# Kernel tuning notes

Measured on AMD Instinct MI355X. Metric: run time of the kernel, lower is better.

Reference implementation:

```python
import jax, jax.numpy as jnp
import numpy as np

NEG = -1.0e9  # large negative number used for causal masking in the original


def setup_inputs() -> dict:
    key = jax.random.key(0)
    ks = jax.random.split(key, 9)
    B, S, D, H = 4, 4096, 512, 64
    sd = 1.0 / np.sqrt(D)
    sh = 1.0 / np.sqrt(H)
    return {
        "x": jax.random.normal(ks[0], (B, S, D), jnp.float32),
        # nn.Linear(d_model, d_head): stored here as (in, out) matrices
        "Wq": jax.random.normal(ks[1], (D, H), jnp.float32) * sd,
        "bq": jax.random.normal(ks[2], (H,), jnp.float32) * 0.01,
        "Wk": jax.random.normal(ks[3], (D, H), jnp.float32) * sd,
        "bk": jax.random.normal(ks[4], (H,), jnp.float32) * 0.01,
        "Wv": jax.random.normal(ks[5], (D, H), jnp.float32) * sd,
        "bv": jax.random.normal(ks[6], (H,), jnp.float32) * 0.01,
        "Wo": jax.random.normal(ks[7], (H, D), jnp.float32) * sh,
        "bo": jax.random.normal(ks[8], (D,), jnp.float32) * 0.01,
    }


def reference(x, Wq, bq, Wk, bk, Wv, bv, Wo, bo):
    # x: (B, S, D)
    B, S, D = x.shape
    Q = x @ Wq + bq  # (B, S, H)
    K = x @ Wk + bk
    V = x @ Wv + bv
    scores = jnp.einsum("bsh,bth->bst", Q, K)  # (B, S, S)
    # NOTE: original divides by sqrt(scores.shape[-1]) == sqrt(seq_len), not sqrt(d_head)
    scores = scores / jnp.sqrt(jnp.asarray(S, scores.dtype))
    # causal mask: strictly-upper-triangular entries get NEG added
    mask = jnp.triu(jnp.full((S, S), NEG, dtype=scores.dtype), k=1)
    attn = jax.nn.softmax(scores + mask[None, :, :], axis=-1)
    out = jnp.einsum("bst,bth->bsh", attn, V)  # (B, S, H)
    return out @ Wo + bo  # (B, S, D)
```

## Files before the change

### kernel.cpp

```cpp
#include <hip/hip_runtime.h>

#define S_LEN 4096
#define NROWS 16384

typedef __attribute__((ext_vector_type(8))) __bf16 bf16x8;
typedef __attribute__((ext_vector_type(8))) unsigned short ushort8;
typedef __attribute__((ext_vector_type(4))) unsigned short ushort4_t;
typedef __attribute__((ext_vector_type(4))) float floatx4;

__device__ __forceinline__ unsigned short f2bf(float f) {
    union { __bf16 h; unsigned short u; } c;
    c.h = (__bf16)f;
    return c.u;
}

__device__ __forceinline__ float fexp2(float x) {
#if __has_builtin(__builtin_amdgcn_exp2f)
    return __builtin_amdgcn_exp2f(x);
#else
    float r; asm("v_exp_f32 %0, %1" : "=v"(r) : "v"(x)); return r;
#endif
}

__global__ __launch_bounds__(256) void convw_kernel(
    const float* __restrict__ Wq, const float* __restrict__ Wk,
    const float* __restrict__ Wv, const float* __restrict__ Wo,
    unsigned short* __restrict__ WqF, unsigned short* __restrict__ WkF,
    unsigned short* __restrict__ WvF, unsigned short* __restrict__ WoF)
{
    int tid = blockIdx.x * 256 + threadIdx.x;
    {
        const int e = tid & 7, cl = (tid >> 3) & 15, quad = (tid >> 7) & 3;
        const int kc = (tid >> 9) & 15, t = tid >> 13;
        const int n = t * 16 + cl, k = kc * 32 + quad * 8 + e;
        WqF[tid] = f2bf(Wq[k * 64 + n]);
        WkF[tid] = f2bf(Wk[k * 64 + n]);
        WvF[tid] = f2bf(Wv[k * 64 + n]);
    }
    {
        const int e = tid & 7, cl = (tid >> 3) & 15, quad = (tid >> 7) & 3;
        const int h = (tid >> 9) & 1, g = tid >> 10;
        const int n = g * 16 + cl, k = h * 32 + quad * 8 + e;
        WoF[tid] = f2bf(Wo[k * 512 + n]);
    }
}

__global__ __launch_bounds__(192) void qkv_kernel(
    const float* __restrict__ x,
    const unsigned short* __restrict__ WqF, const unsigned short* __restrict__ WkF,
    const unsigned short* __restrict__ WvF,
    const float* __restrict__ bq, const float* __restrict__ bk, const float* __restrict__ bv,
    unsigned short* __restrict__ Qb, unsigned short* __restrict__ KF,
    unsigned short* __restrict__ VF)
{
    __shared__ unsigned short xs[8192];
    const int row0 = blockIdx.x * 16;
    const int tid = threadIdx.x;

    const float* xt = x + (size_t)row0 * 512;
    for (int i = tid; i < 2048; i += 192) {
        float4 v = *(const float4*)(xt + i * 4);
        const int r = i >> 7, k = (i & 127) * 4;
        ushort4_t o;
        o[0] = f2bf(v.x); o[1] = f2bf(v.y); o[2] = f2bf(v.z); o[3] = f2bf(v.w);
        *(ushort4_t*)(xs + (k >> 5) * 512 + ((k >> 3) & 3) * 128 + r * 8 + (k & 7)) = o;
    }
    __syncthreads();

    const int m = tid >> 6;
    const int lane = tid & 63, cl = lane & 15, quad = lane >> 4;
    const unsigned short* WF = (m == 0) ? WqF : (m == 1) ? WkF : WvF;
    const float* bias = (m == 0) ? bq : (m == 1) ? bk : bv;

    floatx4 acc[4];
    #pragma unroll
    for (int t = 0; t < 4; t++) acc[t] = (floatx4){0.f, 0.f, 0.f, 0.f};
    #pragma unroll 2
    for (int kc = 0; kc < 16; kc++) {
        const bf16x8 af = *(const bf16x8*)(const void*)(xs + kc * 512 + lane * 8);
        #pragma unroll
        for (int t = 0; t < 4; t++) {
            const bf16x8 bf = *(const bf16x8*)(const void*)(WF + (size_t)(t * 16 + kc) * 512 + lane * 8);
            acc[t] = __builtin_amdgcn_mfma_f32_16x16x32_bf16(af, bf, acc[t], 0, 0, 0);
        }
    }
    if (m == 0) {
        const float scl = 0.022542110013890054f;
        #pragma unroll
        for (int t = 0; t < 4; t++) {
            const int d = t * 16 + cl;
            const float bd = bias[d];
            #pragma unroll
            for (int r = 0; r < 4; r++)
                Qb[(size_t)(row0 + quad * 4 + r) * 64 + d] = f2bf((acc[t][r] + bd) * scl);
        }
    } else if (m == 1) {
        const int g16 = row0 >> 4;
        #pragma unroll
        for (int t = 0; t < 4; t++) {
            const int d = t * 16 + cl;
            const float bd = bias[d];
            const size_t base = ((size_t)g16 * 8 + (d >> 3)) * 128 + (d & 7);
            #pragma unroll
            for (int r = 0; r < 4; r++)
                KF[base + (quad * 4 + r) * 8] = f2bf(acc[t][r] + bd);
        }
    } else {
        const int b = row0 >> 12, s_base = row0 & 4095;
        #pragma unroll
        for (int t = 0; t < 4; t++) {
            const int d = t * 16 + cl;
            const float bd = bias[d];
            #pragma unroll
            for (int r = 0; r < 4; r++) {
                const int s = s_base + quad * 4 + r;
                const size_t off = (size_t)b * (S_LEN * 64) + (size_t)(s >> 6) * 4096
                                 + ((s >> 5) & 1) * 2048 + t * 512 + cl * 32
                                 + ((s >> 3) & 3) * 8 + (s & 7);
                VF[off] = f2bf(acc[t][r] + bd);
            }
        }
    }
}

#define PSTR 152
__global__ __launch_bounds__(256, 2) void attn_kernel(
    const unsigned short* __restrict__ Qb, const unsigned short* __restrict__ Kb,
    const unsigned short* __restrict__ Vt,
    float* __restrict__ Po, float* __restrict__ Pl)
{
    __shared__ float4 shraw[4][304];
    const int bid = blockIdx.x;
    const int pair = bid >> 2, h = bid & 3;
    const int a = 63 - (pair >> 2);
    const int b = pair & 3;
    const int q0 = a * 64;
    const int nkt = a + 1;
    const int kt0 = (h * nkt) >> 2;
    const int kt1 = ((h + 1) * nkt) >> 2;
    const int tid = threadIdx.x;
    const int w = tid >> 6, lane = tid & 63, cl = lane & 15, quad = lane >> 4;

    const size_t qrow = (size_t)b * S_LEN + q0 + w * 16 + cl;
    const bf16x8 aq0 = *(const bf16x8*)(const void*)(Qb + qrow * 64 + quad * 8);
    const bf16x8 aq1 = *(const bf16x8*)(const void*)(Qb + qrow * 64 + 32 + quad * 8);
    const unsigned short* kbb = Kb + (size_t)b * S_LEN * 64;
    const unsigned short* vbb = Vt + (size_t)b * S_LEN * 64;
    const int qm = q0 + w * 16 + quad * 4;

    float lrow[4];
    floatx4 Oacc[4];
    #pragma unroll
    for (int r = 0; r < 4; r++) lrow[r] = 0.f;
    #pragma unroll
    for (int u = 0; u < 4; u++) Oacc[u] = (floatx4){0.f, 0.f, 0.f, 0.f};

    unsigned short* Pw = (unsigned short*)&shraw[w][0];

    int jt = kt0;
    for (; jt + 1 < kt1; jt += 2) {
        float z[8][4];
        bf16x8 vf[8][2];
        {
            bf16x8 kf[4][2];
            #pragma unroll
            for (int t = 0; t < 4; t++) {
                const unsigned short* kp = kbb + ((size_t)(jt * 4 + t) * 8 + quad) * 128 + cl * 8;
                kf[t][0] = *(const bf16x8*)(const void*)kp;
                kf[t][1] = *(const bf16x8*)(const void*)(kp + 512);
            }
            #pragma unroll
            for (int t = 0; t < 4; t++) {
                floatx4 acc = (floatx4){0.f, 0.f, 0.f, 0.f};
                acc = __builtin_amdgcn_mfma_f32_16x16x32_bf16(aq0, kf[t][0], acc, 0, 0, 0);
                acc = __builtin_amdgcn_mfma_f32_16x16x32_bf16(aq1, kf[t][1], acc, 0, 0, 0);
                #pragma unroll
                for (int r = 0; r < 4; r++) z[t][r] = acc[r];
            }
        }
        #pragma unroll
        for (int u = 0; u < 4; u++) {
            const unsigned short* vp = vbb + (size_t)jt * 4096 + u * 512 + cl * 32 + quad * 8;
            vf[u][0] = *(const bf16x8*)(const void*)vp;
            vf[u][1] = *(const bf16x8*)(const void*)(vp + 2048);
        }
        {
            bf16x8 kf[4][2];
            #pragma unroll
            for (int t = 0; t < 4; t++) {
                const unsigned short* kp = kbb + ((size_t)((jt + 1) * 4 + t) * 8 + quad) * 128 + cl * 8;
                kf[t][0] = *(const bf16x8*)(const void*)kp;
                kf[t][1] = *(const bf16x8*)(const void*)(kp + 512);
            }
            #pragma unroll
            for (int t = 0; t < 4; t++) {
                floatx4 acc = (floatx4){0.f, 0.f, 0.f, 0.f};
                acc = __builtin_amdgcn_mfma_f32_16x16x32_bf16(aq0, kf[t][0], acc, 0, 0, 0);
                acc = __builtin_amdgcn_mfma_f32_16x16x32_bf16(aq1, kf[t][1], acc, 0, 0, 0);
                #pragma unroll
                for (int r = 0; r < 4; r++) z[4 + t][r] = acc[r];
            }
        }
        #pragma unroll
        for (int u = 0; u < 4; u++) {
            const unsigned short* vp = vbb + (size_t)(jt + 1) * 4096 + u * 512 + cl * 32 + quad * 8;
            vf[4 + u][0] = *(const bf16x8*)(const void*)vp;
            vf[4 + u][1] = *(const bf16x8*)(const void*)(vp + 2048);
        }
        if (jt + 1 == nkt - 1) {
            const int j0b = (jt + 1) * 64;
            #pragma unroll
            for (int t = 0; t < 4; t++)
                #pragma unroll
                for (int r = 0; r < 4; r++)
                    if (j0b + t * 16 + cl > qm + r) z[4 + t][r] = -1e30f;
        }
        #pragma unroll
        for (int t = 0; t < 8; t++)
            #pragma unroll
            for (int r = 0; r < 4; r++) z[t][r] = fexp2(z[t][r]);
        #pragma unroll
        for (int r = 0; r < 4; r++)
            lrow[r] += ((z[0][r] + z[1][r]) + (z[2][r] + z[3][r]))
                     + ((z[4][r] + z[5][r]) + (z[6][r] + z[7][r]));
        #pragma unroll
        for (int t = 0; t < 8; t++)
            #pragma unroll
            for (int r = 0; r < 4; r++)
                Pw[(quad * 4 + r) * PSTR + t * 16 + cl] = f2bf(z[t][r]);
        bf16x8 ap0 = *(const bf16x8*)(const void*)(Pw + cl * PSTR + quad * 8);
        bf16x8 ap1 = *(const bf16x8*)(const void*)(Pw + cl * PSTR + 32 + quad * 8);
        bf16x8 ap2 = *(const bf16x8*)(const void*)(Pw + cl * PSTR + 64 + quad * 8);
        bf16x8 ap3 = *(const bf16x8*)(const void*)(Pw + cl * PSTR + 96 + quad * 8);
        #pragma unroll
        for (int u = 0; u < 4; u++) {
            Oacc[u] = __builtin_amdgcn_mfma_f32_16x16x32_bf16(ap0, vf[u][0], Oacc[u], 0, 0, 0);
            Oacc[u] = __builtin_amdgcn_mfma_f32_16x16x32_bf16(ap1, vf[u][1], Oacc[u], 0, 0, 0);
            Oacc[u] = __builtin_amdgcn_mfma_f32_16x16x32_bf16(ap2, vf[4 + u][0], Oacc[u], 0, 0, 0);
            Oacc[u] = __builtin_amdgcn_mfma_f32_16x16x32_bf16(ap3, vf[4 + u][1], Oacc[u], 0, 0, 0);
        }
    }
    if (jt < kt1) {
        bf16x8 kf[4][2], vf[4][2];
        #pragma unroll
        for (int t = 0; t < 4; t++) {
            const unsigned short* kp = kbb + ((size_t)(jt * 4 + t) * 8 + quad) * 128 + cl * 8;
            kf[t][0] = *(const bf16x8*)(const void*)kp;
            kf[t][1] = *(const bf16x8*)(const void*)(kp + 512);
        }
        #pragma unroll
        for (int u = 0; u < 4; u++) {
            const unsigned short* vp = vbb + (size_t)jt * 4096 + u * 512 + cl * 32 + quad * 8;
            vf[u][0] = *(const bf16x8*)(const void*)vp;
            vf[u][1] = *(const bf16x8*)(const void*)(vp + 2048);
        }
        float z[4][4];
        #pragma unroll
        for (int t = 0; t < 4; t++) {
            floatx4 acc = (floatx4){0.f, 0.f, 0.f, 0.f};
            acc = __builtin_amdgcn_mfma_f32_16x16x32_bf16(aq0, kf[t][0], acc, 0, 0, 0);
            acc = __builtin_amdgcn_mfma_f32_16x16x32_bf16(aq1, kf[t][1], acc, 0, 0, 0);
            #pragma unroll
            for (int r = 0; r < 4; r++) z[t][r] = acc[r];
        }
        if (jt == nkt - 1) {
            const int j0 = jt * 64;
            #pragma unroll
            for (int t = 0; t < 4; t++)
                #pragma unroll
                for (int r = 0; r < 4; r++)
                    if (j0 + t * 16 + cl > qm + r) z[t][r] = -1e30f;
        }
        #pragma unroll
        for (int t = 0; t < 4; t++)
            #pragma unroll
            for (int r = 0; r < 4; r++) z[t][r] = fexp2(z[t][r]);
        #pragma unroll
        for (int r = 0; r < 4; r++)
            lrow[r] += ((z[0][r] + z[1][r]) + (z[2][r] + z[3][r]));
        #pragma unroll
        for (int t = 0; t < 4; t++)
            #pragma unroll
            for (int r = 0; r < 4; r++)
                Pw[(quad * 4 + r) * PSTR + t * 16 + cl] = f2bf(z[t][r]);
        bf16x8 ap0 = *(const bf16x8*)(const void*)(Pw + cl * PSTR + quad * 8);
        bf16x8 ap1 = *(const bf16x8*)(const void*)(Pw + cl * PSTR + 32 + quad * 8);
        #pragma unroll
        for (int u = 0; u < 4; u++) {
            Oacc[u] = __builtin_amdgcn_mfma_f32_16x16x32_bf16(ap0, vf[u][0], Oacc[u], 0, 0, 0);
            Oacc[u] = __builtin_amdgcn_mfma_f32_16x16x32_bf16(ap1, vf[u][1], Oacc[u], 0, 0, 0);
        }
    }
    #pragma unroll
    for (int r = 0; r < 4; r++) {
        float s = lrow[r];
        s += __shfl_xor(s, 1, 64);
        s += __shfl_xor(s, 2, 64);
        s += __shfl_xor(s, 4, 64);
        s += __shfl_xor(s, 8, 64);
        lrow[r] = s;
    }
    {
        float* pob = Po + (size_t)bid * 4096 + w * 1024;
        #pragma unroll
        for (int u = 0; u < 4; u++) {
            const int base = (u >> 1) * 512
                           + (((u & 1) * 2 + (cl >> 3)) * 16 + quad * 4) * 8 + (cl & 7);
            #pragma unroll
            for (int r = 0; r < 4; r++)
                pob[base + r * 8] = Oacc[u][r];
        }
        if (cl == 0) {
            #pragma unroll
            for (int r = 0; r < 4; r++)
                Pl[(size_t)bid * 64 + w * 16 + quad * 4 + r] = lrow[r];
        }
    }
}

__global__ __launch_bounds__(256) void oproj_kernel(
    const float* __restrict__ Po, const float* __restrict__ Pl,
    const unsigned short* __restrict__ WoF,
    const float* __restrict__ bo, float* __restrict__ out)
{
    const int blk = blockIdx.x;
    const int row0 = blk * 16;
    const int b = row0 >> 12, s0 = row0 & 4095;
    const int a = s0 >> 6, g16 = (s0 >> 4) & 3;
    const int pair = (63 - a) * 4 + b;
    const int tid = threadIdx.x;
    const int w = tid >> 6, lane = tid & 63, cl = lane & 15, quad = lane >> 4;

    float s0v[8], s1v[8];
    #pragma unroll
    for (int e = 0; e < 8; e++) { s0v[e] = 0.f; s1v[e] = 0.f; }
    #pragma unroll
    for (int h = 0; h < 4; h++) {
        const float* p = Po + ((size_t)(pair * 4 + h) * 4 + g16) * 1024 + lane * 8;
        #pragma unroll
        for (int e = 0; e < 8; e++) s0v[e] += p[e];
        #pragma unroll
        for (int e = 0; e < 8; e++) s1v[e] += p[512 + e];
    }
    float L = 0.f;
    #pragma unroll
    for (int h = 0; h < 4; h++)
        L += Pl[(size_t)(pair * 4 + h) * 64 + g16 * 16 + cl];
    const float invL = 1.0f / L;

    bf16x8 a0, a1;
    #pragma unroll
    for (int e = 0; e < 8; e++) {
        a0[e] = (__bf16)(s0v[e] * invL);
        a1[e] = (__bf16)(s1v[e] * invL);
    }

    #pragma unroll 2
    for (int i = 0; i < 8; i++) {
        const int g = w * 8 + i;
        const int n = g * 16 + cl;
        bf16x8 b0 = *(const bf16x8*)(const void*)(WoF + (size_t)(g * 2 + 0) * 512 + lane * 8);
        bf16x8 b1 = *(const bf16x8*)(const void*)(WoF + (size_t)(g * 2 + 1) * 512 + lane * 8);
        floatx4 acc = (floatx4){0.f, 0.f, 0.f, 0.f};
        acc = __builtin_amdgcn_mfma_f32_16x16x32_bf16(a0, b0, acc, 0, 0, 0);
        acc = __builtin_amdgcn_mfma_f32_16x16x32_bf16(a1, b1, acc, 0, 0, 0);
        const float bod = bo[n];
        #pragma unroll
        for (int r = 0; r < 4; r++)
            out[(size_t)(row0 + quad * 4 + r) * 512 + n] = acc[r] + bod;
    }
}

extern "C" void kernel_launch(void* const* d_in, const int* in_sizes, int n_in,
                              void* d_out, int out_size, void* d_ws, size_t ws_size,
                              hipStream_t stream) {
    const float* x  = (const float*)d_in[0];
    const float* Wq = (const float*)d_in[1];
    const float* bq = (const float*)d_in[2];
    const float* Wk = (const float*)d_in[3];
    const float* bk = (const float*)d_in[4];
    const float* Wv = (const float*)d_in[5];
    const float* bv = (const float*)d_in[6];
    const float* Wo = (const float*)d_in[7];
    const float* bo = (const float*)d_in[8];
    float* out = (float*)d_out;

    unsigned short* Qb  = (unsigned short*)d_ws;
    unsigned short* KF  = Qb + (size_t)NROWS * 64;
    unsigned short* VF  = KF + (size_t)NROWS * 64;
    unsigned short* WqF = VF + (size_t)NROWS * 64;
    unsigned short* WkF = WqF + 512 * 64;
    unsigned short* WvF = WkF + 512 * 64;
    unsigned short* WoF = WvF + 512 * 64;
    float* Pl = (float*)(WoF + 512 * 64);
    float* Po = Pl + (size_t)1024 * 64;

    convw_kernel<<<128, 256, 0, stream>>>(Wq, Wk, Wv, Wo, WqF, WkF, WvF, WoF);
    qkv_kernel<<<1024, 192, 0, stream>>>(x, WqF, WkF, WvF, bq, bk, bv, Qb, KF, VF);
    attn_kernel<<<1024, 256, 0, stream>>>(Qb, KF, VF, Po, Pl);
    oproj_kernel<<<NROWS / 16, 256, 0, stream>>>(Po, Pl, WoF, bo, out);
}
```

Measured before the change: 146.9 us.

## Stage K/V tiles through double-buffered LDS shared across waves

Each wave previously loaded the full K and V tiles directly from global memory into registers, so all four waves in a block read the same data redundantly. The new loop has the waves cooperatively copy each 64-key K/V tile into a double-buffered LDS region once, prefetching the next tile into registers while computing on the current one. MFMA operands are then read from LDS. The two-tile unrolled loop becomes a one-tile loop, and the per-wave P scratch stride is halved. This adds a block-wide barrier per tile and more LDS use (about 34 KB per block), which may limit occupancy.

New measurement: 162.1 us. 1.1x slower.

```diff
diff --git a/kernel.cpp b/kernel.cpp
--- a/kernel.cpp
+++ b/kernel.cpp
@@ -123,13 +123,14 @@
     }
 }
 
-#define PSTR 152
+#define PSTR 76
 __global__ __launch_bounds__(256, 2) void attn_kernel(
     const unsigned short* __restrict__ Qb, const unsigned short* __restrict__ Kb,
     const unsigned short* __restrict__ Vt,
     float* __restrict__ Po, float* __restrict__ Pl)
 {
-    __shared__ float4 shraw[4][304];
+    __shared__ float4 kvraw[2][1024];
+    __shared__ float4 psraw[4][152];
     const int bid = blockIdx.x;
     const int pair = bid >> 2, h = bid & 3;
     const int a = 63 - (pair >> 2);
@@ -144,8 +145,8 @@
     const size_t qrow = (size_t)b * S_LEN + q0 + w * 16 + cl;
     const bf16x8 aq0 = *(const bf16x8*)(const void*)(Qb + qrow * 64 + quad * 8);
     const bf16x8 aq1 = *(const bf16x8*)(const void*)(Qb + qrow * 64 + 32 + quad * 8);
-    const unsigned short* kbb = Kb + (size_t)b * S_LEN * 64;
-    const unsigned short* vbb = Vt + (size_t)b * S_LEN * 64;
+    const unsigned short* gkv = ((w < 2) ? Kb : Vt) + (size_t)b * S_LEN * 64
+                              + (w & 1) * 2048 + lane * 8;
     const int qm = q0 + w * 16 + quad * 4;
 
     float lrow[4];
@@ -155,111 +156,38 @@
     #pragma unroll
     for (int u = 0; u < 4; u++) Oacc[u] = (floatx4){0.f, 0.f, 0.f, 0.f};
 
-    unsigned short* Pw = (unsigned short*)&shraw[w][0];
-
-    int jt = kt0;
-    for (; jt + 1 < kt1; jt += 2) {
-        float z[8][4];
-        bf16x8 vf[8][2];
-        {
-            bf16x8 kf[4][2];
-            #pragma unroll
-            for (int t = 0; t < 4; t++) {
-                const unsigned short* kp = kbb + ((size_t)(jt * 4 + t) * 8 + quad) * 128 + cl * 8;
-                kf[t][0] = *(const bf16x8*)(const void*)kp;
-                kf[t][1] = *(const bf16x8*)(const void*)(kp + 512);
-            }
-            #pragma unroll
-            for (int t = 0; t < 4; t++) {
-                floatx4 acc = (floatx4){0.f, 0.f, 0.f, 0.f};
-                acc = __builtin_amdgcn_mfma_f32_16x16x32_bf16(aq0, kf[t][0], acc, 0, 0, 0);
-                acc = __builtin_amdgcn_mfma_f32_16x16x32_bf16(aq1, kf[t][1], acc, 0, 0, 0);
-                #pragma unroll
-                for (int r = 0; r < 4; r++) z[t][r] = acc[r];
-            }
-        }
-        #pragma unroll
-        for (int u = 0; u < 4; u++) {
-            const unsigned short* vp = vbb + (size_t)jt * 4096 + u * 512 + cl * 32 + quad * 8;
-            vf[u][0] = *(const bf16x8*)(const void*)vp;
-            vf[u][1] = *(const bf16x8*)(const void*)(vp + 2048);
-        }
-        {
-            bf16x8 kf[4][2];
-            #pragma unroll
-            for (int t = 0; t < 4; t++) {
-                const unsigned short* kp = kbb + ((size_t)((jt + 1) * 4 + t) * 8 + quad) * 128 + cl * 8;
-                kf[t][0] = *(const bf16x8*)(const void*)kp;
-                kf[t][1] = *(const bf16x8*)(const void*)(kp + 512);
-            }
-            #pragma unroll
-            for (int t = 0; t < 4; t++) {
-                floatx4 acc = (floatx4){0.f, 0.f, 0.f, 0.f};
-                acc = __builtin_amdgcn_mfma_f32_16x16x32_bf16(aq0, kf[t][0], acc, 0, 0, 0);
-                acc = __builtin_amdgcn_mfma_f32_16x16x32_bf16(aq1, kf[t][1], acc, 0, 0, 0);
-                #pragma unroll
-                for (int r = 0; r < 4; r++) z[4 + t][r] = acc[r];
-            }
-        }
-        #pragma unroll
-        for (int u = 0; u < 4; u++) {
-            const unsigned short* vp = vbb + (size_t)(jt + 1) * 4096 + u * 512 + cl * 32 + quad * 8;
-            vf[4 + u][0] = *(const bf16x8*)(const void*)vp;
-            vf[4 + u][1] = *(const bf16x8*)(const void*)(vp + 2048);
-        }
-        if (jt + 1 == nkt - 1) {
-            const int j0b = (jt + 1) * 64;
-            #pragma unroll
-            for (int t = 0; t < 4; t++)
-                #pragma unroll
-                for (int r = 0; r < 4; r++)
-                    if (j0b + t * 16 + cl > qm + r) z[4 + t][r] = -1e30f;
-        }
-        #pragma unroll
-        for (int t = 0; t < 8; t++)
-            #pragma unroll
-            for (int r = 0; r < 4; r++) z[t][r] = fexp2(z[t][r]);
-        #pragma unroll
-        for (int r = 0; r < 4; r++)
-            lrow[r] += ((z[0][r] + z[1][r]) + (z[2][r] + z[3][r]))
-                     + ((z[4][r] + z[5][r]) + (z[6][r] + z[7][r]));
-        #pragma unroll
-        for (int t = 0; t < 8; t++)
-            #pragma unroll
-            for (int r = 0; r < 4; r++)
-                Pw[(quad * 4 + r) * PSTR + t * 16 + cl] = f2bf(z[t][r]);
-        bf16x8 ap0 = *(const bf16x8*)(const void*)(Pw + cl * PSTR + quad * 8);
-        bf16x8 ap1 = *(const bf16x8*)(const void*)(Pw + cl * PSTR + 32 + quad * 8);
-        bf16x8 ap2 = *(const bf16x8*)(const void*)(Pw + cl * PSTR + 64 + quad * 8);
-        bf16x8 ap3 = *(const bf16x8*)(const void*)(Pw + cl * PSTR + 96 + quad * 8);
-        #pragma unroll
-        for (int u = 0; u < 4; u++) {
-            Oacc[u] = __builtin_amdgcn_mfma_f32_16x16x32_bf16(ap0, vf[u][0], Oacc[u], 0, 0, 0);
-            Oacc[u] = __builtin_amdgcn_mfma_f32_16x16x32_bf16(ap1, vf[u][1], Oacc[u], 0, 0, 0);
-            Oacc[u] = __builtin_amdgcn_mfma_f32_16x16x32_bf16(ap2, vf[4 + u][0], Oacc[u], 0, 0, 0);
-            Oacc[u] = __builtin_amdgcn_mfma_f32_16x16x32_bf16(ap3, vf[4 + u][1], Oacc[u], 0, 0, 0);
-        }
-    }
-    if (jt < kt1) {
-        bf16x8 kf[4][2], vf[4][2];
-        #pragma unroll
-        for (int t = 0; t < 4; t++) {
-            const unsigned short* kp = kbb + ((size_t)(jt * 4 + t) * 8 + quad) * 128 + cl * 8;
-            kf[t][0] = *(const bf16x8*)(const void*)kp;
-            kf[t][1] = *(const bf16x8*)(const void*)(kp + 512);
-        }
-        #pragma unroll
-        for (int u = 0; u < 4; u++) {
-            const unsigned short* vp = vbb + (size_t)jt * 4096 + u * 512 + cl * 32 + quad * 8;
-            vf[u][0] = *(const bf16x8*)(const void*)vp;
-            vf[u][1] = *(const bf16x8*)(const void*)(vp + 2048);
-        }
+    unsigned short* Pw = (unsigned short*)&psraw[w][0];
+    const int stg_off = (w >> 1) * 4096 + (w & 1) * 2048 + lane * 8;
+
+    if (kt0 < kt1) {
+        const unsigned short* src = gkv + (size_t)kt0 * 4096;
+        unsigned short* dst = (unsigned short*)&kvraw[0][0] + stg_off;
+        #pragma unroll
+        for (int j = 0; j < 4; j++)
+            *(float4*)(void*)(dst + j * 512) = *(const float4*)(const void*)(src + j * 512);
+    }
+    __syncthreads();
+
+    int cur = 0;
+    for (int jt = kt0; jt < kt1; ++jt) {
+        float4 stg[4];
+        const bool more = (jt + 1 < kt1);
+        if (more) {
+            const unsigned short* src = gkv + (size_t)(jt + 1) * 4096;
+            #pragma unroll
+            for (int j = 0; j < 4; j++)
+                stg[j] = *(const float4*)(const void*)(src + j * 512);
+        }
+        const unsigned short* Ks = (const unsigned short*)&kvraw[cur][0];
+        const unsigned short* Vs = Ks + 4096;
         float z[4][4];
         #pragma unroll
         for (int t = 0; t < 4; t++) {
+            const bf16x8 k0 = *(const bf16x8*)(const void*)(Ks + t * 1024 + quad * 128 + cl * 8);
+            const bf16x8 k1 = *(const bf16x8*)(const void*)(Ks + t * 1024 + quad * 128 + cl * 8 + 512);
             floatx4 acc = (floatx4){0.f, 0.f, 0.f, 0.f};
-            acc = __builtin_amdgcn_mfma_f32_16x16x32_bf16(aq0, kf[t][0], acc, 0, 0, 0);
-            acc = __builtin_amdgcn_mfma_f32_16x16x32_bf16(aq1, kf[t][1], acc, 0, 0, 0);
+            acc = __builtin_amdgcn_mfma_f32_16x16x32_bf16(aq0, k0, acc, 0, 0, 0);
+            acc = __builtin_amdgcn_mfma_f32_16x16x32_bf16(aq1, k1, acc, 0, 0, 0);
             #pragma unroll
             for (int r = 0; r < 4; r++) z[t][r] = acc[r];
         }
@@ -283,14 +211,25 @@
             #pragma unroll
             for (int r = 0; r < 4; r++)
                 Pw[(quad * 4 + r) * PSTR + t * 16 + cl] = f2bf(z[t][r]);
-        bf16x8 ap0 = *(const bf16x8*)(const void*)(Pw + cl * PSTR + quad * 8);
-        bf16x8 ap1 = *(const bf16x8*)(const void*)(Pw + cl * PSTR + 32 + quad * 8);
+        const bf16x8 ap0 = *(const bf16x8*)(const void*)(Pw + cl * PSTR + quad * 8);
+        const bf16x8 ap1 = *(const bf16x8*)(const void*)(Pw + cl * PSTR + 32 + quad * 8);
         #pragma unroll
         for (int u = 0; u < 4; u++) {
-            Oacc[u] = __builtin_amdgcn_mfma_f32_16x16x32_bf16(ap0, vf[u][0], Oacc[u], 0, 0, 0);
-            Oacc[u] = __builtin_amdgcn_mfma_f32_16x16x32_bf16(ap1, vf[u][1], Oacc[u], 0, 0, 0);
-        }
-    }
+            const bf16x8 v0 = *(const bf16x8*)(const void*)(Vs + u * 512 + cl * 32 + quad * 8);
+            const bf16x8 v1 = *(const bf16x8*)(const void*)(Vs + u * 512 + cl * 32 + quad * 8 + 2048);
+            Oacc[u] = __builtin_amdgcn_mfma_f32_16x16x32_bf16(ap0, v0, Oacc[u], 0, 0, 0);
+            Oacc[u] = __builtin_amdgcn_mfma_f32_16x16x32_bf16(ap1, v1, Oacc[u], 0, 0, 0);
+        }
+        if (more) {
+            unsigned short* dst = (unsigned short*)&kvraw[cur ^ 1][0] + stg_off;
+            #pragma unroll
+            for (int j = 0; j < 4; j++)
+                *(float4*)(void*)(dst + j * 512) = stg[j];
+        }
+        __syncthreads();
+        cur ^= 1;
+    }
+
     #pragma unroll
     for (int r = 0; r < 4; r++) {
         float s = lrow[r];
```
